# Kernel tuning notes

Hardware: AMD Instinct MI355X
Metric: run time of the kernel (lower is better)

The kernel has to match this reference:

```python
import jax, jax.numpy as jnp
import numpy as np

B, T, N, C, H, S = 8, 24, 2048, 64, 8, 4
HD = C // H
EPS_NORM = 1e-12   # torch F.normalize eps
EPS_DEN = 1e-5     # clamp_min in fast_attention
LN_EPS = 1e-5
SCALE1 = 0.01      # self.scale[1]


def _ln(x, g, b):
    m = x.mean(-1, keepdims=True)
    v = ((x - m) ** 2).mean(-1, keepdims=True)
    return (x - m) * jax.lax.rsqrt(v + LN_EPS) * g + b


def _fast_attn(q, k, v):
    # q,k,v: [b, l, h, m] ; performer-style linear attention with L2-normalized feature maps
    q = q / jnp.maximum(jnp.linalg.norm(q, axis=-1, keepdims=True), EPS_NORM)
    k = k / jnp.maximum(jnp.linalg.norm(k, axis=-1, keepdims=True), EPS_NORM)
    L = q.shape[1]
    kvs = jnp.einsum('blhm,blhd->bhmd', k, v)
    num = jnp.einsum('bnhm,bhmd->bnhd', q, kvs) + L * v
    den = jnp.einsum('bnhm,bhm->bnh', q, k.sum(axis=1))[..., None] + L
    return num / jnp.maximum(den, EPS_DEN)  # [b, l, h, d]


def _attn_layer(x, qkv_w, out_w, out_b):
    # x: [B, T, N, C]; spatial (over N) + temporal (over T) linear attention, concat, project
    b, t, n, c = x.shape
    qkv = x @ qkv_w.T                      # [b,t,n,3c], no bias (qkv_bias=False)
    q, k, v = jnp.split(qkv, 3, axis=-1)
    sh = lambda a: a.reshape(b * t, n, H, HD)                    # flatten (B,T) -> attend over nodes
    th = lambda a: a.swapaxes(1, 2).reshape(b * n, t, H, HD)     # flatten (B,N) -> attend over time
    out_s = _fast_attn(sh(q), sh(k), sh(v)).reshape(b, t, n, c)
    out_t = _fast_attn(th(q), th(k), th(v)).reshape(b, n, t, c).swapaxes(1, 2)
    return jnp.concatenate([out_s, out_t], axis=-1) @ out_w.T + out_b


def setup_inputs() -> dict:
    key = jax.random.key(0)
    ks = jax.random.split(key, 20)
    stdv = 1.0 / np.sqrt(N)
    w = 0.02
    inp = {
        'x': jax.random.normal(ks[0], (B, T, N, C), jnp.float32),
        'phi': jax.random.normal(ks[1], (S, N, N), jnp.float32) * (N ** -0.5),
        'phi_inv': jax.random.normal(ks[2], (S, N, N), jnp.float32) * (N ** -0.5),
        'diag_w': jax.random.uniform(ks[3], (S, N), jnp.float32, -stdv, stdv),
        'qkv0_w': jax.random.normal(ks[4], (3 * C, C), jnp.float32) * w,
        'out0_w': jax.random.normal(ks[5], (C, 2 * C), jnp.float32) * w,
        'out0_b': jnp.zeros((C,), jnp.float32),
        'qkv1_w': jax.random.normal(ks[6], (3 * C, C), jnp.float32) * w,
        'out1_w': jax.random.normal(ks[7], (C, 2 * C), jnp.float32) * w,
        'out1_b': jnp.zeros((C,), jnp.float32),
        'pw0_w': jax.random.normal(ks[8], (C, C), jnp.float32) * w,
        'pw0_b': jax.random.normal(ks[9], (C,), jnp.float32) * w,
        'pw1_w': jax.random.normal(ks[10], (C, C), jnp.float32) * w,
        'pw1_b': jax.random.normal(ks[11], (C,), jnp.float32) * w,
        'fc1_w': jax.random.normal(ks[12], (2 * C, C), jnp.float32) * w,
        'fc1_b': jnp.zeros((2 * C,), jnp.float32),
        'fc2_w': jax.random.normal(ks[13], (C, 2 * C), jnp.float32) * w,
        'fc2_b': jnp.zeros((C,), jnp.float32),
        'ln1_g': jnp.ones((C,), jnp.float32),
        'ln1_b': jnp.zeros((C,), jnp.float32),
        'ln2_g': jnp.ones((C,), jnp.float32),
        'ln2_b': jnp.zeros((C,), jnp.float32),
    }
    return inp


def reference(x, phi, phi_inv, diag_w, qkv0_w, out0_w, out0_b, qkv1_w, out1_w, out1_b,
              pw0_w, pw0_b, pw1_w, pw1_b, fc1_w, fc1_b, fc2_w, fc2_b,
              ln1_g, ln1_b, ln2_g, ln2_b):
    # Graph wavelet propagate (order=2): x_list = [x, W(x)] with
    # W(x)[b,t,n,c] = sum_j (sum_s phi_s diag(diag_w_s) phi_inv_s)[n,j] x[b,t,j,c]
    Msum = jnp.einsum('sij,sj,sjk->ik', phi, diag_w, phi_inv)   # [N,N]
    x_k = jnp.einsum('nj,btjc->btnc', Msum, x)
    att0 = _attn_layer(x, qkv0_w, out0_w, out0_b)
    att1 = _attn_layer(x_k, qkv1_w, out1_w, out1_b)
    # scale = [1, 0.01]; c starts as x, then becomes att0
    x_glo = x + att0 * (x @ pw0_w.T + pw0_b) + att1 * (att0 @ pw1_w.T + pw1_b) * SCALE1
    # In torch, x_glo aliases x (in-place +=), so ln1(x + x_glo) == ln1(2 * x_glo)
    y = _ln(2.0 * x_glo, ln1_g, ln1_b)
    h = jax.nn.relu(y @ fc1_w.T + fc1_b) @ fc2_w.T + fc2_b
    return _ln(y + h, ln2_g, ln2_b)
```

## Files before the change

kernel.cpp:

```cpp
#include <hip/hip_runtime.h>

typedef unsigned short u16;
typedef unsigned int u32;
typedef __attribute__((ext_vector_type(8))) __bf16 bf16x8;
typedef __attribute__((ext_vector_type(4))) float floatx4;

#define TB 24
#define NN 2048
#define QC 192

__device__ __forceinline__ float b2f(u16 v) { return __uint_as_float(((u32)v) << 16); }
__device__ __forceinline__ u16 f2bu(float f) {
  u32 u = __float_as_uint(f);
  u32 r = (u + 0x7fffu + ((u >> 16) & 1u)) >> 16;
  return (u16)r;
}
__device__ __forceinline__ u32 packpair(float a, float b) {
  return (u32)f2bu(a) | ((u32)f2bu(b) << 16);
}
__device__ __forceinline__ void unpack8(uint4 v, float* f) {
  f[0] = __uint_as_float(v.x << 16); f[1] = __uint_as_float(v.x & 0xffff0000u);
  f[2] = __uint_as_float(v.y << 16); f[3] = __uint_as_float(v.y & 0xffff0000u);
  f[4] = __uint_as_float(v.z << 16); f[5] = __uint_as_float(v.z & 0xffff0000u);
  f[6] = __uint_as_float(v.w << 16); f[7] = __uint_as_float(v.w & 0xffff0000u);
}
__device__ __forceinline__ float wredsum(float v) {
#pragma unroll
  for (int m = 32; m > 0; m >>= 1) v += __shfl_xor(v, m, 64);
  return v;
}
__device__ __forceinline__ float red16(float v) {
#pragma unroll
  for (int m = 8; m > 0; m >>= 1) v += __shfl_xor(v, m, 64);
  return v;
}

__global__ __launch_bounds__(256) void cast_weights(
    const float* __restrict__ q0, const float* __restrict__ q1,
    const float* __restrict__ o0, const float* __restrict__ o1,
    const float* __restrict__ p0, const float* __restrict__ p1,
    const float* __restrict__ f1, const float* __restrict__ f2,
    u16* __restrict__ dst) {
  int i = blockIdx.x * 256 + threadIdx.x;
  float v;
  if (i < 12288) v = q0[i];
  else if (i < 24576) v = q1[i - 12288];
  else if (i < 32768) v = o0[i - 24576];
  else if (i < 40960) v = o1[i - 32768];
  else if (i < 45056) v = p0[i - 40960];
  else if (i < 49152) v = p1[i - 45056];
  else if (i < 57344) v = f1[i - 49152];
  else v = f2[i - 57344];
  dst[i] = f2bu(v);
}

__global__ __launch_bounds__(256) void cast_bulk(const float* __restrict__ src,
                                                 u16* __restrict__ dst) {
  long i = ((long)blockIdx.x * 256 + threadIdx.x) * 8;
  float4 a = *(const float4*)(src + i);
  float4 b = *(const float4*)(src + i + 4);
  uint4 o = uint4{packpair(a.x, a.y), packpair(a.z, a.w),
                  packpair(b.x, b.y), packpair(b.z, b.w)};
  *(uint4*)(dst + i) = o;
}

__global__ __launch_bounds__(256) void prep_pt(const float* __restrict__ phi_inv,
                                               const float* __restrict__ diag,
                                               u16* __restrict__ PT) {
  const int s = blockIdx.z;
  const float* phi_inv_s = phi_inv + (long)s * 4194304;
  const float* diag_s = diag + (long)s * 2048;
  u16* PTs = PT + (long)s * 4194304;
  const long i0 = (long)blockIdx.x * 64, j0 = (long)blockIdx.y * 64;
  __shared__ float tile[64][65];
  for (int t = threadIdx.x; t < 512; t += 256) {
    int r = t >> 3, c8 = (t & 7) << 3;
    float dv = diag_s[j0 + r];
    const float* sp = phi_inv_s + (j0 + r) * 2048 + i0 + c8;
    float4 p = *(const float4*)sp;
    float4 q = *(const float4*)(sp + 4);
    tile[r][c8 + 0] = p.x * dv; tile[r][c8 + 1] = p.y * dv;
    tile[r][c8 + 2] = p.z * dv; tile[r][c8 + 3] = p.w * dv;
    tile[r][c8 + 4] = q.x * dv; tile[r][c8 + 5] = q.y * dv;
    tile[r][c8 + 6] = q.z * dv; tile[r][c8 + 7] = q.w * dv;
  }
  __syncthreads();
  for (int t = threadIdx.x; t < 512; t += 256) {
    int r = t >> 3, c8 = (t & 7) << 3;
    uint4 o;
    o.x = packpair(tile[c8 + 0][r], tile[c8 + 1][r]);
    o.y = packpair(tile[c8 + 2][r], tile[c8 + 3][r]);
    o.z = packpair(tile[c8 + 4][r], tile[c8 + 5][r]);
    o.w = packpair(tile[c8 + 6][r], tile[c8 + 7][r]);
    *(uint4*)(PTs + (i0 + r) * 2048 + j0 + c8) = o;
  }
}

__global__ __launch_bounds__(256) void prep_xt(const float* __restrict__ x,
                                               u16* __restrict__ XT,
                                               u16* __restrict__ XB) {
  const int bt = blockIdx.y;
  const long j0 = (long)blockIdx.x * 64;
  __shared__ float tile[64][65];
  const float* src = x + (long)bt * NN * 64;
  for (int t = threadIdx.x; t < 512; t += 256) {
    int r = t >> 3, c8 = (t & 7) << 3;
    const float* sp = src + (j0 + r) * 64 + c8;
    float4 p = *(const float4*)sp;
    float4 q = *(const float4*)(sp + 4);
    tile[r][c8 + 0] = p.x; tile[r][c8 + 1] = p.y;
    tile[r][c8 + 2] = p.z; tile[r][c8 + 3] = p.w;
    tile[r][c8 + 4] = q.x; tile[r][c8 + 5] = q.y;
    tile[r][c8 + 6] = q.z; tile[r][c8 + 7] = q.w;
    if (XB) {
      uint4 o = uint4{packpair(p.x, p.y), packpair(p.z, p.w),
                      packpair(q.x, q.y), packpair(q.z, q.w)};
      *(uint4*)(XB + (long)bt * 131072 + (j0 + r) * 64 + c8) = o;
    }
  }
  __syncthreads();
  u16* dst = XT + (long)bt * 64 * NN;
  for (int t = threadIdx.x; t < 512; t += 256) {
    int r = t >> 3, c8 = (t & 7) << 3;
    uint4 o;
    o.x = packpair(tile[c8 + 0][r], tile[c8 + 1][r]);
    o.y = packpair(tile[c8 + 2][r], tile[c8 + 3][r]);
    o.z = packpair(tile[c8 + 4][r], tile[c8 + 5][r]);
    o.w = packpair(tile[c8 + 6][r], tile[c8 + 7][r]);
    *(uint4*)(dst + (long)r * 2048 + j0 + c8) = o;
  }
}

template <int MODE>
__global__ __launch_bounds__(256) void gemm128(
    const u16* __restrict__ A, const u16* __restrict__ Bt, void* __restrict__ C,
    int K, int lda, int ldb, int ldc, int nseg, long aseg, long bseg) {
  __shared__ __align__(16) u16 As[128 * 64];
  __shared__ __align__(16) u16 Bs[128 * 64];
  const int tid = threadIdx.x;
  const int wave = tid >> 6, lane = tid & 63;
  const int l15 = lane & 15, lq = lane >> 4;
  const int wr = wave >> 1, wc = wave & 1;
  const int nbx = gridDim.x;
  const int nwg = nbx * gridDim.y;
  int id = blockIdx.x + nbx * blockIdx.y;
  id = (id & 7) * (nwg >> 3) + (id >> 3);
  const long m0 = (long)(id % nbx) * 128;
  const long n0 = (long)(id / nbx) * 128;
  const long zo = (MODE == 2) ? (long)blockIdx.z : 0;
  const int rl = lane >> 3;
  const int csw = (lane & 7) ^ rl;
  floatx4 acc[4][4];
#pragma unroll
  for (int a = 0; a < 4; a++)
#pragma unroll
    for (int b = 0; b < 4; b++) acc[a][b] = floatx4{0.f, 0.f, 0.f, 0.f};
  for (int s = 0; s < nseg; s++) {
    const u16* Ab = A + (s + zo) * aseg;
    const u16* Bb = Bt + (s + zo) * bseg;
    for (int k0 = 0; k0 < K; k0 += 64) {
      __syncthreads();
#pragma unroll
      for (int la = 0; la < 4; la++) {
        const int ldx = wave * 4 + la;
        const int rowt = ldx * 8 + rl;
        const u16* ga = Ab + (m0 + rowt) * (long)lda + k0 + csw * 8;
        const u16* gb = Bb + (n0 + rowt) * (long)ldb + k0 + csw * 8;
        __builtin_amdgcn_global_load_lds(
            (const __attribute__((address_space(1))) void*)ga,
            (__attribute__((address_space(3))) void*)(As + ldx * 512), 16, 0, 0);
        __builtin_amdgcn_global_load_lds(
            (const __attribute__((address_space(1))) void*)gb,
            (__attribute__((address_space(3))) void*)(Bs + ldx * 512), 16, 0, 0);
      }
      __syncthreads();
#pragma unroll
      for (int ks = 0; ks < 2; ks++) {
        bf16x8 af[4], bf[4];
        const int cp = ((ks * 4 + lq) ^ (l15 & 7)) * 8;
#pragma unroll
        for (int t = 0; t < 4; t++) {
          af[t] = *(const bf16x8*)(As + (wr * 64 + t * 16 + l15) * 64 + cp);
          bf[t] = *(const bf16x8*)(Bs + (wc * 64 + t * 16 + l15) * 64 + cp);
        }
#pragma unroll
        for (int ti = 0; ti < 4; ti++)
#pragma unroll
          for (int tj = 0; tj < 4; tj++)
            acc[ti][tj] = __builtin_amdgcn_mfma_f32_16x16x32_bf16(
                af[ti], bf[tj], acc[ti][tj], 0, 0, 0);
      }
    }
  }
#pragma unroll
  for (int ti = 0; ti < 4; ti++) {
#pragma unroll
    for (int tj = 0; tj < 4; tj++) {
#pragma unroll
      for (int i = 0; i < 4; i++) {
        const long row = m0 + wr * 64 + ti * 16 + lq * 4 + i;
        const long col = n0 + wc * 64 + tj * 16 + l15;
        if (MODE == 0) {
          ((u16*)C)[row * ldc + col] = f2bu(acc[ti][tj][i]);
        } else if (MODE == 1) {
          ((float*)C)[(col >> 6) * 131072L + row * 64 + (col & 63)] = acc[ti][tj][i];
        } else if (MODE == 2) {
          ((float*)C)[zo * 4194304L + row * (long)ldc + col] = acc[ti][tj][i];
        } else {
          ((u16*)C)[(col >> 6) * 131072L + row * 64 + (col & 63)] =
              f2bu(acc[ti][tj][i]);
        }
      }
    }
  }
}

__global__ __launch_bounds__(256) void reduce_ms(const float* __restrict__ P,
                                                 u16* __restrict__ M) {
  long i = ((long)blockIdx.x * 256 + threadIdx.x) * 8;
  float s[8];
  {
    float4 a = *(const float4*)(P + i);
    float4 b = *(const float4*)(P + i + 4);
    s[0] = a.x; s[1] = a.y; s[2] = a.z; s[3] = a.w;
    s[4] = b.x; s[5] = b.y; s[6] = b.z; s[7] = b.w;
  }
#pragma unroll
  for (int z = 1; z < 4; z++) {
    const float* p = P + (long)z * 4194304L + i;
    float4 a = *(const float4*)p;
    float4 b = *(const float4*)(p + 4);
    s[0] += a.x; s[1] += a.y; s[2] += a.z; s[3] += a.w;
    s[4] += b.x; s[5] += b.y; s[6] += b.z; s[7] += b.w;
  }
  uint4 o = uint4{packpair(s[0], s[1]), packpair(s[2], s[3]),
                  packpair(s[4], s[5]), packpair(s[6], s[7])};
  *(uint4*)(M + i) = o;
}

template <bool AF32, bool CF32>
__global__ __launch_bounds__(256) void gemm_bt(
    const void* __restrict__ A, const u16* __restrict__ Bt, void* __restrict__ C,
    int K, int lda, int ldb, int ldc, int nseg, long aseg, long bseg,
    long bbstride, long cbstride, int accum) {
  __shared__ __align__(16) u16 Asm[64][72];
  __shared__ __align__(16) u16 Bsm[64][72];
  const int tid = threadIdx.x;
  const int wave = tid >> 6, lane = tid & 63;
  const int l15 = lane & 15, lq = lane >> 4;
  const long m0 = (long)blockIdx.x * 64;
  const long n0 = (long)blockIdx.y * 64;
  const long bz = blockIdx.z;
  const int srow = tid >> 3;
  const int scol = (tid & 7) << 3;
  floatx4 acc[4];
#pragma unroll
  for (int t = 0; t < 4; t++) acc[t] = floatx4{0.f, 0.f, 0.f, 0.f};
  for (int s = 0; s < nseg; s++) {
    const u16* Bb = Bt + s * bseg + bz * bbstride;
    for (int k0 = 0; k0 < K; k0 += 64) {
      __syncthreads();
      uint4 a0, a1;
      if (AF32) {
        const float* Af = (const float*)A + s * aseg;
        const float* p0 = Af + (m0 + srow) * lda + k0 + scol;
        const float* p1 = Af + (m0 + srow + 32) * lda + k0 + scol;
        float4 x0 = *(const float4*)p0, x1 = *(const float4*)(p0 + 4);
        float4 y0 = *(const float4*)p1, y1 = *(const float4*)(p1 + 4);
        a0 = uint4{packpair(x0.x, x0.y), packpair(x0.z, x0.w),
                   packpair(x1.x, x1.y), packpair(x1.z, x1.w)};
        a1 = uint4{packpair(y0.x, y0.y), packpair(y0.z, y0.w),
                   packpair(y1.x, y1.y), packpair(y1.z, y1.w)};
      } else {
        const u16* Ab = (const u16*)A + s * aseg;
        a0 = *(const uint4*)(Ab + (m0 + srow) * lda + k0 + scol);
        a1 = *(const uint4*)(Ab + (m0 + srow + 32) * lda + k0 + scol);
      }
      uint4 b0 = *(const uint4*)(Bb + (n0 + srow) * ldb + k0 + scol);
      uint4 b1 = *(const uint4*)(Bb + (n0 + srow + 32) * ldb + k0 + scol);
      *(uint4*)(&Asm[srow][scol]) = a0;
      *(uint4*)(&Asm[srow + 32][scol]) = a1;
      *(uint4*)(&Bsm[srow][scol]) = b0;
      *(uint4*)(&Bsm[srow + 32][scol]) = b1;
      __syncthreads();
#pragma unroll
      for (int ks = 0; ks < 2; ks++) {
        bf16x8 af = *(const bf16x8*)(&Asm[wave * 16 + l15][ks * 32 + lq * 8]);
#pragma unroll
        for (int t = 0; t < 4; t++) {
          bf16x8 bfr = *(const bf16x8*)(&Bsm[t * 16 + l15][ks * 32 + lq * 8]);
          acc[t] = __builtin_amdgcn_mfma_f32_16x16x32_bf16(af, bfr, acc[t], 0, 0, 0);
        }
      }
    }
  }
#pragma unroll
  for (int t = 0; t < 4; t++) {
#pragma unroll
    for (int i = 0; i < 4; i++) {
      long off = (m0 + wave * 16 + lq * 4 + i) * ldc + n0 + t * 16 + l15;
      float v = acc[t][i];
      if (CF32) {
        float* Cb = (float*)C + bz * cbstride;
        if (accum) v += Cb[off];
        Cb[off] = v;
      } else {
        u16* Cb = (u16*)C + bz * cbstride;
        if (accum) v += b2f(Cb[off]);
        Cb[off] = f2bu(v);
      }
    }
  }
}

template <int K, int LDA, int NOUT, int LDO, bool BIAS, bool RELU, bool AF32, bool OF32>
__global__ __launch_bounds__(256) void skinny_gemm(const void* __restrict__ In,
                                                   const u16* __restrict__ W,
                                                   const float* __restrict__ Bv,
                                                   void* __restrict__ Out) {
  constexpr int NT = NOUT / 16;
  const int lane = threadIdx.x & 63;
  const int wave = threadIdx.x >> 6;
  const int l15 = lane & 15, lq = lane >> 4;
  const long m0 = ((long)blockIdx.x * 4 + wave) * 16;
  floatx4 acc[NT];
#pragma unroll
  for (int t = 0; t < NT; t++) acc[t] = floatx4{0.f, 0.f, 0.f, 0.f};
#pragma unroll
  for (int k0 = 0; k0 < K; k0 += 32) {
    bf16x8 af;
    if (AF32) {
      const float* arow = (const float*)In + (m0 + l15) * (long)LDA + lq * 8;
      float4 p = *(const float4*)(arow + k0);
      float4 q = *(const float4*)(arow + k0 + 4);
      uint4 pk = uint4{packpair(p.x, p.y), packpair(p.z, p.w),
                       packpair(q.x, q.y), packpair(q.z, q.w)};
      af = __builtin_bit_cast(bf16x8, pk);
    } else {
      const u16* arow = (const u16*)In + (m0 + l15) * (long)LDA + lq * 8;
      af = *(const bf16x8*)(arow + k0);
    }
#pragma unroll
    for (int t = 0; t < NT; t++) {
      bf16x8 bfr = *(const bf16x8*)(W + (t * 16 + l15) * K + k0 + lq * 8);
      acc[t] = __builtin_amdgcn_mfma_f32_16x16x32_bf16(af, bfr, acc[t], 0, 0, 0);
    }
  }
#pragma unroll
  for (int t = 0; t < NT; t++) {
    float bv = BIAS ? Bv[t * 16 + l15] : 0.f;
#pragma unroll
    for (int i = 0; i < 4; i++) {
      float v = acc[t][i] + bv;
      if (RELU) v = fmaxf(v, 0.f);
      long off = (m0 + lq * 4 + i) * (long)LDO + t * 16 + l15;
      if (OF32) ((float*)Out)[off] = v;
      else ((u16*)Out)[off] = f2bu(v);
    }
  }
}

__global__ __launch_bounds__(256) void spat_stats(const u16* __restrict__ Q,
                                                  float* __restrict__ stats) {
  const int nb = gridDim.x;
  int blk = blockIdx.x;
  const int bh = ((nb & 7) == 0) ? ((blk & 7) * (nb >> 3) + (blk >> 3)) : blk;
  const int bt = bh >> 3, h = bh & 7;
  const int tid = threadIdx.x, lane = tid & 63, wave = tid >> 6;
  float kvs[8][8], ksm[8];
#pragma unroll
  for (int m = 0; m < 8; m++) {
    ksm[m] = 0.f;
#pragma unroll
    for (int d = 0; d < 8; d++) kvs[m][d] = 0.f;
  }
  const u16* base = Q + (long)bt * NN * QC + 64 + h * 8;
  for (int l = tid; l < NN; l += 256) {
    const u16* p = base + (long)l * QC;
    float kv[8], vv[8];
    unpack8(*(const uint4*)p, kv);
    unpack8(*(const uint4*)(p + 64), vv);
    float nr = 0.f;
#pragma unroll
    for (int m = 0; m < 8; m++) nr += kv[m] * kv[m];
    float inv = 1.f / fmaxf(sqrtf(nr), 1e-12f);
#pragma unroll
    for (int m = 0; m < 8; m++) {
      float km = kv[m] * inv;
      ksm[m] += km;
#pragma unroll
      for (int d = 0; d < 8; d++) kvs[m][d] += km * vv[d];
    }
  }
  __shared__ float red[4][72];
#pragma unroll
  for (int m = 0; m < 8; m++) {
    ksm[m] = wredsum(ksm[m]);
#pragma unroll
    for (int d = 0; d < 8; d++) kvs[m][d] = wredsum(kvs[m][d]);
  }
  if (lane == 0) {
#pragma unroll
    for (int m = 0; m < 8; m++) {
      red[wave][64 + m] = ksm[m];
#pragma unroll
      for (int d = 0; d < 8; d++) red[wave][m * 8 + d] = kvs[m][d];
    }
  }
  __syncthreads();
  if (tid < 72) {
    stats[(long)bh * 72 + tid] = red[0][tid] + red[1][tid] + red[2][tid] + red[3][tid];
  }
}

__global__ __launch_bounds__(256) void temp_attn(u16* __restrict__ Q) {
  const long g = (long)blockIdx.x * 256 + threadIdx.x;
  const int h = (int)(g & 7);
  const long bn = g >> 3;
  const int n = (int)(bn & 2047);
  const int b = (int)(bn >> 11);
  u16* qb = Q + ((long)b * TB * NN + n) * QC + h * 8;
  const long ts = (long)NN * QC;
  float kvs[8][8], ksm[8];
#pragma unroll
  for (int m = 0; m < 8; m++) {
    ksm[m] = 0.f;
#pragma unroll
    for (int d = 0; d < 8; d++) kvs[m][d] = 0.f;
  }
  for (int t = 0; t < TB; t++) {
    const u16* p = qb + t * ts;
    float kv[8], vv[8];
    unpack8(*(const uint4*)(p + 64), kv);
    unpack8(*(const uint4*)(p + 128), vv);
    float nr = 0.f;
#pragma unroll
    for (int m = 0; m < 8; m++) nr += kv[m] * kv[m];
    float inv = 1.f / fmaxf(sqrtf(nr), 1e-12f);
#pragma unroll
    for (int m = 0; m < 8; m++) {
      float km = kv[m] * inv;
      ksm[m] += km;
#pragma unroll
      for (int d = 0; d < 8; d++) kvs[m][d] += km * vv[d];
    }
  }
  for (int t = 0; t < TB; t++) {
    u16* p = qb + t * ts;
    float qv[8], vv[8];
    unpack8(*(const uint4*)p, qv);
    unpack8(*(const uint4*)(p + 128), vv);
    float nr = 0.f;
#pragma unroll
    for (int m = 0; m < 8; m++) nr += qv[m] * qv[m];
    float inv = 1.f / fmaxf(sqrtf(nr), 1e-12f);
    float num[8];
    float den = 24.f;
#pragma unroll
    for (int d = 0; d < 8; d++) num[d] = 24.f * vv[d];
#pragma unroll
    for (int m = 0; m < 8; m++) {
      float qm = qv[m] * inv;
      den += qm * ksm[m];
#pragma unroll
      for (int d = 0; d < 8; d++) num[d] += qm * kvs[m][d];
    }
    den = fmaxf(den, 1e-5f);
    float id = 1.f / den;
    uint4 o;
    o.x = packpair(num[0] * id, num[1] * id);
    o.y = packpair(num[2] * id, num[3] * id);
    o.z = packpair(num[4] * id, num[5] * id);
    o.w = packpair(num[6] * id, num[7] * id);
    *(uint4*)(p + 64) = o;
  }
}

__global__ __launch_bounds__(256) void temp_spat(u16* __restrict__ Q,
                                                 const float* __restrict__ stats) {
  const long g = (long)blockIdx.x * 256 + threadIdx.x;
  const int h = (int)(g & 7);
  const long bn = g >> 3;
  const int n = (int)(bn & 2047);
  const int b = (int)(bn >> 11);
  u16* qb = Q + ((long)b * TB * NN + n) * QC + h * 8;
  const long ts = (long)NN * QC;
  float kvs[8][8], ksm[8];
#pragma unroll
  for (int m = 0; m < 8; m++) {
    ksm[m] = 0.f;
#pragma unroll
    for (int d = 0; d < 8; d++) kvs[m][d] = 0.f;
  }
  for (int t = 0; t < TB; t++) {
    const u16* p = qb + t * ts;
    float kv[8], vv[8];
    unpack8(*(const uint4*)(p + 64), kv);
    unpack8(*(const uint4*)(p + 128), vv);
    float nr = 0.f;
#pragma unroll
    for (int m = 0; m < 8; m++) nr += kv[m] * kv[m];
    float inv = 1.f / fmaxf(sqrtf(nr), 1e-12f);
#pragma unroll
    for (int m = 0; m < 8; m++) {
      float km = kv[m] * inv;
      ksm[m] += km;
#pragma unroll
      for (int d = 0; d < 8; d++) kvs[m][d] += km * vv[d];
    }
  }
  const float* stb = stats + ((long)b * TB * 8 + h) * 72;
  for (int t = 0; t < TB; t++) {
    u16* p = qb + t * ts;
    const float* st = stb + (long)t * 576;
    float qv[8], vv[8];
    unpack8(*(const uint4*)p, qv);
    unpack8(*(const uint4*)(p + 128), vv);
    float nr = 0.f;
#pragma unroll
    for (int m = 0; m < 8; m++) nr += qv[m] * qv[m];
    float inv = 1.f / fmaxf(sqrtf(nr), 1e-12f);
    float numt[8], nums[8];
    float dent = 24.f, dens = 2048.f;
#pragma unroll
    for (int d = 0; d < 8; d++) {
      numt[d] = 24.f * vv[d];
      nums[d] = 2048.f * vv[d];
    }
#pragma unroll
    for (int m = 0; m < 8; m++) {
      float qm = qv[m] * inv;
      dent += qm * ksm[m];
      dens += qm * st[64 + m];
#pragma unroll
      for (int d = 0; d < 8; d++) {
        numt[d] += qm * kvs[m][d];
        nums[d] += qm * st[m * 8 + d];
      }
    }
    float idt = 1.f / fmaxf(dent, 1e-5f);
    float ids = 1.f / fmaxf(dens, 1e-5f);
    uint4 os, ot;
    os.x = packpair(nums[0] * ids, nums[1] * ids);
    os.y = packpair(nums[2] * ids, nums[3] * ids);
    os.z = packpair(nums[4] * ids, nums[5] * ids);
    os.w = packpair(nums[6] * ids, nums[7] * ids);
    ot.x = packpair(numt[0] * idt, numt[1] * idt);
    ot.y = packpair(numt[2] * idt, numt[3] * idt);
    ot.z = packpair(numt[4] * idt, numt[5] * idt);
    ot.w = packpair(numt[6] * idt, numt[7] * idt);
    *(uint4*)p = os;
    *(uint4*)(p + 64) = ot;
  }
}

__global__ __launch_bounds__(256) void spat_out(u16* __restrict__ Q,
                                                const float* __restrict__ stats) {
  const long g = (long)blockIdx.x * 256 + threadIdx.x;
  const int h = (int)(g & 7);
  const long r = g >> 3;
  const int bt = (int)(r >> 11);
  u16* p = Q + r * QC + h * 8;
  float qv[8], vv[8];
  unpack8(*(const uint4*)p, qv);
  unpack8(*(const uint4*)(p + 128), vv);
  const float* st = stats + ((long)bt * 8 + h) * 72;
  float nr = 0.f;
#pragma unroll
  for (int m = 0; m < 8; m++) nr += qv[m] * qv[m];
  float inv = 1.f / fmaxf(sqrtf(nr), 1e-12f);
  const float L = 2048.f;
  float num[8];
#pragma unroll
  for (int d = 0; d < 8; d++) num[d] = L * vv[d];
  float den = L;
#pragma unroll
  for (int m = 0; m < 8; m++) {
    float qm = qv[m] * inv;
    den += qm * st[64 + m];
#pragma unroll
    for (int d = 0; d < 8; d++) num[d] += qm * st[m * 8 + d];
  }
  den = fmaxf(den, 1e-5f);
  float id = 1.f / den;
  uint4 o;
  o.x = packpair(num[0] * id, num[1] * id);
  o.y = packpair(num[2] * id, num[3] * id);
  o.z = packpair(num[4] * id, num[5] * id);
  o.w = packpair(num[6] * id, num[7] * id);
  *(uint4*)p = o;
}

__global__ __launch_bounds__(256) void pw1_combine_ln(
    const u16* __restrict__ Q, const u16* __restrict__ W,
    const float* __restrict__ Bv, const float* __restrict__ x,
    const u16* __restrict__ a1, const float* __restrict__ g1,
    const float* __restrict__ b1, u16* __restrict__ Y) {
  const int lane = threadIdx.x & 63;
  const int wave = threadIdx.x >> 6;
  const int l15 = lane & 15, lq = lane >> 4;
  const long m0 = ((long)blockIdx.x * 4 + wave) * 16;
  floatx4 acc[4];
#pragma unroll
  for (int t = 0; t < 4; t++) acc[t] = floatx4{0.f, 0.f, 0.f, 0.f};
#pragma unroll
  for (int k0 = 0; k0 < 64; k0 += 32) {
    bf16x8 af = *(const bf16x8*)(Q + (m0 + l15) * 192 + 128 + k0 + lq * 8);
#pragma unroll
    for (int t = 0; t < 4; t++) {
      bf16x8 bfr = *(const bf16x8*)(W + (t * 16 + l15) * 64 + k0 + lq * 8);
      acc[t] = __builtin_amdgcn_mfma_f32_16x16x32_bf16(af, bfr, acc[t], 0, 0, 0);
    }
  }
  float tv[4][4];
#pragma unroll
  for (int t = 0; t < 4; t++) {
    const int col = t * 16 + l15;
    const float bv = Bv[col];
#pragma unroll
    for (int i = 0; i < 4; i++) {
      const long row = m0 + lq * 4 + i;
      float p1v = acc[t][i] + bv;
      float xv = x[row * 64 + col];
      float a0 = b2f(Q[row * 192 + 128 + col]);
      float p0 = b2f(Q[row * 192 + col]);
      float a1v = b2f(a1[row * 64 + col]);
      tv[t][i] = 2.f * (xv + a0 * p0 + a1v * p1v * 0.01f);
    }
  }
#pragma unroll
  for (int i = 0; i < 4; i++) {
    float s = tv[0][i] + tv[1][i] + tv[2][i] + tv[3][i];
    s = red16(s);
    float mu = s * 0.015625f;
    float vs = 0.f;
#pragma unroll
    for (int t = 0; t < 4; t++) {
      float d = tv[t][i] - mu;
      vs += d * d;
    }
    vs = red16(vs);
    float rs = rsqrtf(vs * 0.015625f + 1e-5f);
    const long row = m0 + lq * 4 + i;
#pragma unroll
    for (int t = 0; t < 4; t++) {
      const int col = t * 16 + l15;
      float y = (tv[t][i] - mu) * rs * g1[col] + b1[col];
      Y[row * 64 + col] = f2bu(y);
    }
  }
}

__global__ __launch_bounds__(256) void fc2_ln(
    const u16* __restrict__ Hb, const u16* __restrict__ W,
    const float* __restrict__ Bv, const u16* __restrict__ Yb,
    const float* __restrict__ g2, const float* __restrict__ b2v,
    float* __restrict__ out) {
  const int lane = threadIdx.x & 63;
  const int wave = threadIdx.x >> 6;
  const int l15 = lane & 15, lq = lane >> 4;
  const long m0 = ((long)blockIdx.x * 4 + wave) * 16;
  floatx4 acc[4];
#pragma unroll
  for (int t = 0; t < 4; t++) acc[t] = floatx4{0.f, 0.f, 0.f, 0.f};
#pragma unroll
  for (int k0 = 0; k0 < 128; k0 += 32) {
    bf16x8 af = *(const bf16x8*)(Hb + (m0 + l15) * 128 + k0 + lq * 8);
#pragma unroll
    for (int t = 0; t < 4; t++) {
      bf16x8 bfr = *(const bf16x8*)(W + (t * 16 + l15) * 128 + k0 + lq * 8);
      acc[t] = __builtin_amdgcn_mfma_f32_16x16x32_bf16(af, bfr, acc[t], 0, 0, 0);
    }
  }
  float tv[4][4];
#pragma unroll
  for (int t = 0; t < 4; t++) {
    const int col = t * 16 + l15;
    const float bv = Bv[col];
#pragma unroll
    for (int i = 0; i < 4; i++) {
      const long row = m0 + lq * 4 + i;
      tv[t][i] = acc[t][i] + bv + b2f(Yb[row * 64 + col]);
    }
  }
#pragma unroll
  for (int i = 0; i < 4; i++) {
    float s = tv[0][i] + tv[1][i] + tv[2][i] + tv[3][i];
    s = red16(s);
    float mu = s * 0.015625f;
    float vs = 0.f;
#pragma unroll
    for (int t = 0; t < 4; t++) {
      float d = tv[t][i] - mu;
      vs += d * d;
    }
    vs = red16(vs);
    float rs = rsqrtf(vs * 0.015625f + 1e-5f);
    const long row = m0 + lq * 4 + i;
#pragma unroll
    for (int t = 0; t < 4; t++) {
      const int col = t * 16 + l15;
      out[row * 64 + col] = (tv[t][i] - mu) * rs * g2[col] + b2v[col];
    }
  }
}

__global__ __launch_bounds__(256) void combine_ln(
    const float* __restrict__ x, const u16* __restrict__ a0p, int sa0,
    const float* __restrict__ a1p, const u16* __restrict__ P0, int sp0,
    const u16* __restrict__ P1, int sp1, const float* __restrict__ g1,
    const float* __restrict__ b1, u16* __restrict__ Y) {
  const long r = (long)blockIdx.x * 4 + (threadIdx.x >> 6);
  const int d = threadIdx.x & 63;
  float xv = x[r * 64 + d];
  float a0 = b2f(a0p[r * sa0 + d]);
  float a1 = a1p[r * 64 + d];
  float p0 = b2f(P0[r * sp0 + d]);
  float p1 = b2f(P1[r * sp1 + d]);
  float t = 2.f * (xv + a0 * p0 + a1 * p1 * 0.01f);
  float mu = wredsum(t) * 0.015625f;
  float dv = t - mu;
  float var = wredsum(dv * dv) * 0.015625f;
  float y = dv * rsqrtf(var + 1e-5f) * g1[d] + b1[d];
  Y[r * 64 + d] = f2bu(y);
}

__global__ __launch_bounds__(256) void final_ln(const u16* __restrict__ Yp,
                                                const u16* __restrict__ Op,
                                                const float* __restrict__ g2,
                                                const float* __restrict__ b2p,
                                                float* __restrict__ out) {
  const long r = (long)blockIdx.x * 4 + (threadIdx.x >> 6);
  const int d = threadIdx.x & 63;
  const long o = r * 64 + d;
  float t = b2f(Yp[o]) + b2f(Op[o]);
  float mu = wredsum(t) * 0.015625f;
  float dv = t - mu;
  float var = wredsum(dv * dv) * 0.015625f;
  out[o] = dv * rsqrtf(var + 1e-5f) * g2[d] + b2p[d];
}

extern "C" void kernel_launch(void* const* d_in, const int* in_sizes, int n_in,
                              void* d_out, int out_size, void* d_ws, size_t ws_size,
                              hipStream_t stream) {
  const float* x = (const float*)d_in[0];
  const float* phi = (const float*)d_in[1];
  const float* phiinv = (const float*)d_in[2];
  const float* diagw = (const float*)d_in[3];
  const float* qkv0w = (const float*)d_in[4];
  const float* out0w = (const float*)d_in[5];
  const float* out0b = (const float*)d_in[6];
  const float* qkv1w = (const float*)d_in[7];
  const float* out1w = (const float*)d_in[8];
  const float* out1b = (const float*)d_in[9];
  const float* pw0w = (const float*)d_in[10];
  const float* pw0b = (const float*)d_in[11];
  const float* pw1w = (const float*)d_in[12];
  const float* pw1b = (const float*)d_in[13];
  const float* fc1w = (const float*)d_in[14];
  const float* fc1b = (const float*)d_in[15];
  const float* fc2w = (const float*)d_in[16];
  const float* fc2b = (const float*)d_in[17];
  const float* ln1g = (const float*)d_in[18];
  const float* ln1b = (const float*)d_in[19];
  const float* ln2g = (const float*)d_in[20];
  const float* ln2b = (const float*)d_in[21];

  const long per = 25221120L;
  int CH = 1;
  if ((long)ws_size >= 262144L + 8 * per) CH = 8;
  else if ((long)ws_size >= 262144L + 4 * per) CH = 4;
  else if ((long)ws_size >= 262144L + 2 * per) CH = 2;
  const int NCH = 8 / CH;

  char* ws = (char*)d_ws;
  u16* wb = (u16*)ws;
  u16* wq0 = wb + 0;
  u16* wq1 = wb + 12288;
  u16* wo0 = wb + 24576;
  u16* wo1 = wb + 32768;
  u16* wp0 = wb + 40960;
  u16* wp1 = wb + 45056;
  u16* wf1 = wb + 49152;
  u16* wf2 = wb + 57344;
  const long B0 = 262144L;
  float* dof = (float*)d_out;

  cast_weights<<<256, 256, 0, stream>>>(qkv0w, qkv1w, out0w, out1w, pw0w, pw1w,
                                        fc1w, fc2w, wb);

  if (CH == 8) {
    u16* PT = (u16*)(ws + B0);
    u16* PB = (u16*)(ws + B0 + 33554432L);
    float* MsP = (float*)(ws + B0 + 67108864L);
    u16* Ms = (u16*)(ws + B0 + 134217728L);
    u16* XT = (u16*)(ws + B0);
    u16* XB = (u16*)(ws + B0 + 151437312L);
    u16* Q = (u16*)(ws + B0);
    float* st = (float*)(ws + B0 + 150994944L);
    u16* Yb = XB;
    u16* Hb = (u16*)(ws + B0);
    u16* xkb = (u16*)d_out;
    u16* a1b = xkb + 25165824L;

    prep_pt<<<dim3(32, 32, 4), 256, 0, stream>>>(phiinv, diagw, PT);
    cast_bulk<<<8192, 256, 0, stream>>>(phi, PB);
    gemm128<2><<<dim3(16, 16, 4), 256, 0, stream>>>(PB, PT, MsP, 2048, 2048, 2048,
                                                    2048, 1, 4194304L, 4194304L);
    reduce_ms<<<2048, 256, 0, stream>>>(MsP, Ms);
    prep_xt<<<dim3(32, 192), 256, 0, stream>>>(x, XT, XB);
    gemm128<3><<<dim3(16, 96), 256, 0, stream>>>(Ms, XT, xkb, 2048, 2048, 2048, 0,
                                                 1, 0L, 0L);
    skinny_gemm<64, 64, 192, 192, false, false, false, false>
        <<<6144, 256, 0, stream>>>(xkb, wq1, nullptr, Q);
    spat_stats<<<1536, 256, 0, stream>>>(Q, st);
    temp_spat<<<512, 256, 0, stream>>>(Q, st);
    skinny_gemm<128, 192, 64, 64, true, false, false, false>
        <<<6144, 256, 0, stream>>>(Q, wo1, out1b, a1b);
    skinny_gemm<64, 64, 192, 192, false, false, false, false>
        <<<6144, 256, 0, stream>>>(XB, wq0, nullptr, Q);
    spat_stats<<<1536, 256, 0, stream>>>(Q, st);
    temp_spat<<<512, 256, 0, stream>>>(Q, st);
    skinny_gemm<128, 192, 64, 192, true, false, false, false>
        <<<6144, 256, 0, stream>>>(Q, wo0, out0b, Q + 128);
    skinny_gemm<64, 64, 64, 192, true, false, false, false>
        <<<6144, 256, 0, stream>>>(XB, wp0, pw0b, Q);
    pw1_combine_ln<<<6144, 256, 0, stream>>>(Q, wp1, pw1b, x, a1b, ln1g, ln1b, Yb);
    skinny_gemm<64, 64, 128, 128, true, true, false, false>
        <<<6144, 256, 0, stream>>>(Yb, wf1, fc1b, Hb);
    fc2_ln<<<6144, 256, 0, stream>>>(Hb, wf2, fc2b, Yb, ln2g, ln2b, dof);
  } else {
    u16* Ms = (u16*)(ws + B0);
    u16* PT = (u16*)(ws + B0 + 8388608L);
    u16* XT = (u16*)(ws + B0 + 8388608L);
    u16* Q = (u16*)(ws + B0);
    float* st = (float*)(ws + B0 + (long)CH * 18874368L);
    u16* Yb = (u16*)(ws + B0 + (long)CH * 18929664L);
    u16* Hb = (u16*)(ws + B0);
    u16* Ob = (u16*)(ws + B0 + (long)CH * 12582912L);

    for (int s = 0; s < 4; s++) {
      prep_pt<<<dim3(32, 32, 1), 256, 0, stream>>>(phiinv + (long)s * 4194304,
                                                   diagw + (long)s * 2048, PT);
      gemm_bt<true, false><<<dim3(32, 32, 1), 256, 0, stream>>>(
          phi + (long)s * 4194304, PT, Ms, 2048, 2048, 2048, 2048, 1, 0L, 0L, 0L,
          0L, s ? 1 : 0);
    }
    for (int c = 0; c < NCH; c++) {
      long eoff = (long)c * CH * 49152 * 64;
      prep_xt<<<dim3(32, CH * 24), 256, 0, stream>>>(x + eoff, XT, nullptr);
      gemm_bt<false, true><<<dim3(32, 1, CH * 24), 256, 0, stream>>>(
          Ms, XT, dof + eoff, 2048, 2048, 2048, 64, 1, 0L, 0L, 131072L, 131072L, 0);
    }
    for (int c = 0; c < NCH; c++) {
      long eoff = (long)c * CH * 49152 * 64;
      skinny_gemm<64, 64, 192, 192, false, false, true, false>
          <<<CH * 768, 256, 0, stream>>>(dof + eoff, wq1, nullptr, Q);
      spat_stats<<<CH * 192, 256, 0, stream>>>(Q, st);
      temp_attn<<<CH * 64, 256, 0, stream>>>(Q);
      spat_out<<<CH * 1536, 256, 0, stream>>>(Q, st);
      skinny_gemm<128, 192, 64, 64, true, false, false, true>
          <<<CH * 768, 256, 0, stream>>>(Q, wo1, out1b, dof + eoff);
    }
    for (int c = 0; c < NCH; c++) {
      long eoff = (long)c * CH * 49152 * 64;
      const float* x_c = x + eoff;
      skinny_gemm<64, 64, 192, 192, false, false, true, false>
          <<<CH * 768, 256, 0, stream>>>(x_c, wq0, nullptr, Q);
      spat_stats<<<CH * 192, 256, 0, stream>>>(Q, st);
      temp_attn<<<CH * 64, 256, 0, stream>>>(Q);
      spat_out<<<CH * 1536, 256, 0, stream>>>(Q, st);
      skinny_gemm<128, 192, 64, 192, true, false, false, false>
          <<<CH * 768, 256, 0, stream>>>(Q, wo0, out0b, Q + 128);
      skinny_gemm<64, 64, 64, 192, true, false, true, false>
          <<<CH * 768, 256, 0, stream>>>(x_c, wp0, pw0b, Q);
      skinny_gemm<64, 192, 64, 192, true, false, false, false>
          <<<CH * 768, 256, 0, stream>>>(Q + 128, wp1, pw1b, Q + 64);
      combine_ln<<<CH * 12288, 256, 0, stream>>>(x_c, Q + 128, 192, dof + eoff, Q,
                                                 192, Q + 64, 192, ln1g, ln1b, Yb);
      skinny_gemm<64, 64, 128, 128, true, true, false, false>
          <<<CH * 768, 256, 0, stream>>>(Yb, wf1, fc1b, Hb);
      skinny_gemm<128, 128, 64, 64, true, false, false, false>
          <<<CH * 768, 256, 0, stream>>>(Hb, wf2, fc2b, Ob);
      final_ln<<<CH * 12288, 256, 0, stream>>>(Yb, Ob, ln2g, ln2b, dof + eoff);
    }
  }
}
```

Measured before the change: 1.339 ms.

## Fuse tail GEMMs and LayerNorms into two kernels; remap temp_spat to wave-per-node

Five tail launches (out0 proj, pw0 proj, pw1+combine+LN1, fc1, fc2+LN2) become two kernels that keep intermediates (att0, fc1 hidden) in LDS per wave. This avoids writing and re-reading those activations through global memory. temp_spat now gives each node a whole wave with one output channel per lane, so each thread holds 8 accumulators instead of 72, with 8x more blocks. tail1 writes Y in place over XB, the same buffer it reads; this is safe only because each wave reads its own rows before writing them.

```diff
diff --git a/kernel.cpp b/kernel.cpp
--- a/kernel.cpp
+++ b/kernel.cpp
@@ -413,6 +413,81 @@
   }
 }
 
+__global__ __launch_bounds__(256) void temp_spat(u16* __restrict__ Q,
+                                                 const float* __restrict__ stats) {
+  const int wid = blockIdx.x * 4 + (threadIdx.x >> 6);
+  const int lane = threadIdx.x & 63;
+  const int h = lane >> 3, d = lane & 7;
+  const int n = wid & 2047;
+  const int b = wid >> 11;
+  u16* qb = Q + ((long)b * TB * NN + n) * QC;
+  const long ts = (long)NN * QC;
+  float kvsd[8], ksm[8];
+#pragma unroll
+  for (int m = 0; m < 8; m++) { kvsd[m] = 0.f; ksm[m] = 0.f; }
+  for (int tb = 0; tb < TB; tb += 4) {
+    uint4 kr[4]; u16 vr[4];
+#pragma unroll
+    for (int j = 0; j < 4; j++) {
+      const u16* p = qb + (long)(tb + j) * ts;
+      kr[j] = *(const uint4*)(p + 64 + h * 8);
+      vr[j] = p[128 + lane];
+    }
+#pragma unroll
+    for (int j = 0; j < 4; j++) {
+      float kv[8];
+      unpack8(kr[j], kv);
+      float vvd = b2f(vr[j]);
+      float nr = 0.f;
+#pragma unroll
+      for (int m = 0; m < 8; m++) nr += kv[m] * kv[m];
+      float inv = 1.f / fmaxf(sqrtf(nr), 1e-12f);
+#pragma unroll
+      for (int m = 0; m < 8; m++) {
+        float km = kv[m] * inv;
+        ksm[m] += km;
+        kvsd[m] += km * vvd;
+      }
+    }
+  }
+  const float* stb = stats + ((long)b * TB * 8 + h) * 72;
+  for (int tb = 0; tb < TB; tb += 4) {
+    uint4 qr[4]; u16 vr[4];
+#pragma unroll
+    for (int j = 0; j < 4; j++) {
+      const u16* p = qb + (long)(tb + j) * ts;
+      qr[j] = *(const uint4*)(p + h * 8);
+      vr[j] = p[128 + lane];
+    }
+#pragma unroll
+    for (int j = 0; j < 4; j++) {
+      const float* st = stb + (long)(tb + j) * 576;
+      float qv[8];
+      unpack8(qr[j], qv);
+      float vvd = b2f(vr[j]);
+      float nr = 0.f;
+#pragma unroll
+      for (int m = 0; m < 8; m++) nr += qv[m] * qv[m];
+      float inv = 1.f / fmaxf(sqrtf(nr), 1e-12f);
+      float numt = 24.f * vvd, nums = 2048.f * vvd;
+      float dent = 24.f, dens = 2048.f;
+#pragma unroll
+      for (int m = 0; m < 8; m++) {
+        float qm = qv[m] * inv;
+        dent += qm * ksm[m];
+        dens += qm * st[64 + m];
+        numt += qm * kvsd[m];
+        nums += qm * st[m * 8 + d];
+      }
+      float idt = 1.f / fmaxf(dent, 1e-5f);
+      float ids = 1.f / fmaxf(dens, 1e-5f);
+      u16* p = qb + (long)(tb + j) * ts;
+      p[lane] = f2bu(nums * ids);
+      p[64 + lane] = f2bu(numt * idt);
+    }
+  }
+}
+
 __global__ __launch_bounds__(256) void temp_attn(u16* __restrict__ Q) {
   const long g = (long)blockIdx.x * 256 + threadIdx.x;
   const int h = (int)(g & 7);
@@ -473,84 +548,6 @@
     o.z = packpair(num[4] * id, num[5] * id);
     o.w = packpair(num[6] * id, num[7] * id);
     *(uint4*)(p + 64) = o;
-  }
-}
-
-__global__ __launch_bounds__(256) void temp_spat(u16* __restrict__ Q,
-                                                 const float* __restrict__ stats) {
-  const long g = (long)blockIdx.x * 256 + threadIdx.x;
-  const int h = (int)(g & 7);
-  const long bn = g >> 3;
-  const int n = (int)(bn & 2047);
-  const int b = (int)(bn >> 11);
-  u16* qb = Q + ((long)b * TB * NN + n) * QC + h * 8;
-  const long ts = (long)NN * QC;
-  float kvs[8][8], ksm[8];
-#pragma unroll
-  for (int m = 0; m < 8; m++) {
-    ksm[m] = 0.f;
-#pragma unroll
-    for (int d = 0; d < 8; d++) kvs[m][d] = 0.f;
-  }
-  for (int t = 0; t < TB; t++) {
-    const u16* p = qb + t * ts;
-    float kv[8], vv[8];
-    unpack8(*(const uint4*)(p + 64), kv);
-    unpack8(*(const uint4*)(p + 128), vv);
-    float nr = 0.f;
-#pragma unroll
-    for (int m = 0; m < 8; m++) nr += kv[m] * kv[m];
-    float inv = 1.f / fmaxf(sqrtf(nr), 1e-12f);
-#pragma unroll
-    for (int m = 0; m < 8; m++) {
-      float km = kv[m] * inv;
-      ksm[m] += km;
-#pragma unroll
-      for (int d = 0; d < 8; d++) kvs[m][d] += km * vv[d];
-    }
-  }
-  const float* stb = stats + ((long)b * TB * 8 + h) * 72;
-  for (int t = 0; t < TB; t++) {
-    u16* p = qb + t * ts;
-    const float* st = stb + (long)t * 576;
-    float qv[8], vv[8];
-    unpack8(*(const uint4*)p, qv);
-    unpack8(*(const uint4*)(p + 128), vv);
-    float nr = 0.f;
-#pragma unroll
-    for (int m = 0; m < 8; m++) nr += qv[m] * qv[m];
-    float inv = 1.f / fmaxf(sqrtf(nr), 1e-12f);
-    float numt[8], nums[8];
-    float dent = 24.f, dens = 2048.f;
-#pragma unroll
-    for (int d = 0; d < 8; d++) {
-      numt[d] = 24.f * vv[d];
-      nums[d] = 2048.f * vv[d];
-    }
-#pragma unroll
-    for (int m = 0; m < 8; m++) {
-      float qm = qv[m] * inv;
-      dent += qm * ksm[m];
-      dens += qm * st[64 + m];
-#pragma unroll
-      for (int d = 0; d < 8; d++) {
-        numt[d] += qm * kvs[m][d];
-        nums[d] += qm * st[m * 8 + d];
-      }
-    }
-    float idt = 1.f / fmaxf(dent, 1e-5f);
-    float ids = 1.f / fmaxf(dens, 1e-5f);
-    uint4 os, ot;
-    os.x = packpair(nums[0] * ids, nums[1] * ids);
-    os.y = packpair(nums[2] * ids, nums[3] * ids);
-    os.z = packpair(nums[4] * ids, nums[5] * ids);
-    os.w = packpair(nums[6] * ids, nums[7] * ids);
-    ot.x = packpair(numt[0] * idt, numt[1] * idt);
-    ot.y = packpair(numt[2] * idt, numt[3] * idt);
-    ot.z = packpair(numt[4] * idt, numt[5] * idt);
-    ot.w = packpair(numt[6] * idt, numt[7] * idt);
-    *(uint4*)p = os;
-    *(uint4*)(p + 64) = ot;
   }
 }
 
@@ -591,11 +588,15 @@
   *(uint4*)p = o;
 }
 
-__global__ __launch_bounds__(256) void pw1_combine_ln(
-    const u16* __restrict__ Q, const u16* __restrict__ W,
-    const float* __restrict__ Bv, const float* __restrict__ x,
-    const u16* __restrict__ a1, const float* __restrict__ g1,
-    const float* __restrict__ b1, u16* __restrict__ Y) {
+__global__ __launch_bounds__(256) void tail1(
+    const u16* __restrict__ Q, const u16* __restrict__ XB,
+    const float* __restrict__ x, const u16* __restrict__ a1b,
+    const u16* __restrict__ wo0, const float* __restrict__ o0b,
+    const u16* __restrict__ wp0, const float* __restrict__ p0b,
+    const u16* __restrict__ wp1, const float* __restrict__ p1b,
+    const float* __restrict__ g1, const float* __restrict__ b1,
+    u16* __restrict__ Y) {
+  __shared__ u16 A0[4][16][72];
   const int lane = threadIdx.x & 63;
   const int wave = threadIdx.x >> 6;
   const int l15 = lane & 15, lq = lane >> 4;
@@ -604,28 +605,59 @@
 #pragma unroll
   for (int t = 0; t < 4; t++) acc[t] = floatx4{0.f, 0.f, 0.f, 0.f};
 #pragma unroll
+  for (int k0 = 0; k0 < 128; k0 += 32) {
+    bf16x8 af = *(const bf16x8*)(Q + (m0 + l15) * 192 + k0 + lq * 8);
+#pragma unroll
+    for (int t = 0; t < 4; t++) {
+      bf16x8 bfr = *(const bf16x8*)(wo0 + (t * 16 + l15) * 128 + k0 + lq * 8);
+      acc[t] = __builtin_amdgcn_mfma_f32_16x16x32_bf16(af, bfr, acc[t], 0, 0, 0);
+    }
+  }
+#pragma unroll
+  for (int t = 0; t < 4; t++) {
+    float bv = o0b[t * 16 + l15];
+#pragma unroll
+    for (int i = 0; i < 4; i++)
+      A0[wave][lq * 4 + i][t * 16 + l15] = f2bu(acc[t][i] + bv);
+  }
+  floatx4 ap0[4];
+#pragma unroll
+  for (int t = 0; t < 4; t++) ap0[t] = floatx4{0.f, 0.f, 0.f, 0.f};
+#pragma unroll
   for (int k0 = 0; k0 < 64; k0 += 32) {
-    bf16x8 af = *(const bf16x8*)(Q + (m0 + l15) * 192 + 128 + k0 + lq * 8);
+    bf16x8 af = *(const bf16x8*)(XB + (m0 + l15) * 64 + k0 + lq * 8);
 #pragma unroll
     for (int t = 0; t < 4; t++) {
-      bf16x8 bfr = *(const bf16x8*)(W + (t * 16 + l15) * 64 + k0 + lq * 8);
-      acc[t] = __builtin_amdgcn_mfma_f32_16x16x32_bf16(af, bfr, acc[t], 0, 0, 0);
+      bf16x8 bfr = *(const bf16x8*)(wp0 + (t * 16 + l15) * 64 + k0 + lq * 8);
+      ap0[t] = __builtin_amdgcn_mfma_f32_16x16x32_bf16(af, bfr, ap0[t], 0, 0, 0);
+    }
+  }
+  floatx4 ap1[4];
+#pragma unroll
+  for (int t = 0; t < 4; t++) ap1[t] = floatx4{0.f, 0.f, 0.f, 0.f};
+#pragma unroll
+  for (int k0 = 0; k0 < 64; k0 += 32) {
+    bf16x8 af = *(const bf16x8*)(&A0[wave][l15][k0 + lq * 8]);
+#pragma unroll
+    for (int t = 0; t < 4; t++) {
+      bf16x8 bfr = *(const bf16x8*)(wp1 + (t * 16 + l15) * 64 + k0 + lq * 8);
+      ap1[t] = __builtin_amdgcn_mfma_f32_16x16x32_bf16(af, bfr, ap1[t], 0, 0, 0);
     }
   }
   float tv[4][4];
 #pragma unroll
   for (int t = 0; t < 4; t++) {
     const int col = t * 16 + l15;
-    const float bv = Bv[col];
+    const float bp0 = p0b[col], bp1 = p1b[col];
 #pragma unroll
     for (int i = 0; i < 4; i++) {
       const long row = m0 + lq * 4 + i;
-      float p1v = acc[t][i] + bv;
       float xv = x[row * 64 + col];
-      float a0 = b2f(Q[row * 192 + 128 + col]);
-      float p0 = b2f(Q[row * 192 + col]);
-      float a1v = b2f(a1[row * 64 + col]);
-      tv[t][i] = 2.f * (xv + a0 * p0 + a1v * p1v * 0.01f);
+      float a0 = b2f(A0[wave][lq * 4 + i][col]);
+      float a1 = b2f(a1b[row * 64 + col]);
+      float p0v = ap0[t][i] + bp0;
+      float p1v = ap1[t][i] + bp1;
+      tv[t][i] = 2.f * (xv + a0 * p0v + a1 * p1v * 0.01f);
     }
   }
 #pragma unroll
@@ -636,8 +668,8 @@
     float vs = 0.f;
 #pragma unroll
     for (int t = 0; t < 4; t++) {
-      float d = tv[t][i] - mu;
-      vs += d * d;
+      float dd = tv[t][i] - mu;
+      vs += dd * dd;
     }
     vs = red16(vs);
     float rs = rsqrtf(vs * 0.015625f + 1e-5f);
@@ -651,48 +683,68 @@
   }
 }
 
-__global__ __launch_bounds__(256) void fc2_ln(
-    const u16* __restrict__ Hb, const u16* __restrict__ W,
-    const float* __restrict__ Bv, const u16* __restrict__ Yb,
-    const float* __restrict__ g2, const float* __restrict__ b2v,
-    float* __restrict__ out) {
+__global__ __launch_bounds__(256) void tail2(
+    const u16* __restrict__ Yb, const u16* __restrict__ wf1,
+    const float* __restrict__ f1b, const u16* __restrict__ wf2,
+    const float* __restrict__ fc2bv, const float* __restrict__ g2,
+    const float* __restrict__ b2v, float* __restrict__ out) {
+  __shared__ u16 HL[4][16][136];
   const int lane = threadIdx.x & 63;
   const int wave = threadIdx.x >> 6;
   const int l15 = lane & 15, lq = lane >> 4;
   const long m0 = ((long)blockIdx.x * 4 + wave) * 16;
-  floatx4 acc[4];
-#pragma unroll
-  for (int t = 0; t < 4; t++) acc[t] = floatx4{0.f, 0.f, 0.f, 0.f};
+  floatx4 acc1[8];
+#pragma unroll
+  for (int t = 0; t < 8; t++) acc1[t] = floatx4{0.f, 0.f, 0.f, 0.f};
+#pragma unroll
+  for (int k0 = 0; k0 < 64; k0 += 32) {
+    bf16x8 af = *(const bf16x8*)(Yb + (m0 + l15) * 64 + k0 + lq * 8);
+#pragma unroll
+    for (int t = 0; t < 8; t++) {
+      bf16x8 bfr = *(const bf16x8*)(wf1 + (t * 16 + l15) * 64 + k0 + lq * 8);
+      acc1[t] = __builtin_amdgcn_mfma_f32_16x16x32_bf16(af, bfr, acc1[t], 0, 0, 0);
+    }
+  }
+#pragma unroll
+  for (int t = 0; t < 8; t++) {
+    float bv = f1b[t * 16 + l15];
+#pragma unroll
+    for (int i = 0; i < 4; i++)
+      HL[wave][lq * 4 + i][t * 16 + l15] = f2bu(fmaxf(acc1[t][i] + bv, 0.f));
+  }
+  floatx4 acc2[4];
+#pragma unroll
+  for (int t = 0; t < 4; t++) acc2[t] = floatx4{0.f, 0.f, 0.f, 0.f};
 #pragma unroll
   for (int k0 = 0; k0 < 128; k0 += 32) {
-    bf16x8 af = *(const bf16x8*)(Hb + (m0 + l15) * 128 + k0 + lq * 8);
+    bf16x8 af = *(const bf16x8*)(&HL[wave][l15][k0 + lq * 8]);
 #pragma unroll
     for (int t = 0; t < 4; t++) {
-      bf16x8 bfr = *(const bf16x8*)(W + (t * 16 + l15) * 128 + k0 + lq * 8);
-      acc[t] = __builtin_amdgcn_mfma_f32_16x16x32_bf16(af, bfr, acc[t], 0, 0, 0);
-    }
-  }
-  float tv[4][4];
+      bf16x8 bfr = *(const bf16x8*)(wf2 + (t * 16 + l15) * 128 + k0 + lq * 8);
+      acc2[t] = __builtin_amdgcn_mfma_f32_16x16x32_bf16(af, bfr, acc2[t], 0, 0, 0);
+    }
+  }
+  float tw[4][4];
 #pragma unroll
   for (int t = 0; t < 4; t++) {
     const int col = t * 16 + l15;
-    const float bv = Bv[col];
+    const float bv = fc2bv[col];
 #pragma unroll
     for (int i = 0; i < 4; i++) {
       const long row = m0 + lq * 4 + i;
-      tv[t][i] = acc[t][i] + bv + b2f(Yb[row * 64 + col]);
+      tw[t][i] = acc2[t][i] + bv + b2f(Yb[row * 64 + col]);
     }
   }
 #pragma unroll
   for (int i = 0; i < 4; i++) {
-    float s = tv[0][i] + tv[1][i] + tv[2][i] + tv[3][i];
+    float s = tw[0][i] + tw[1][i] + tw[2][i] + tw[3][i];
     s = red16(s);
     float mu = s * 0.015625f;
     float vs = 0.f;
 #pragma unroll
     for (int t = 0; t < 4; t++) {
-      float d = tv[t][i] - mu;
-      vs += d * d;
+      float dd = tw[t][i] - mu;
+      vs += dd * dd;
     }
     vs = red16(vs);
     float rs = rsqrtf(vs * 0.015625f + 1e-5f);
@@ -700,7 +752,7 @@
 #pragma unroll
     for (int t = 0; t < 4; t++) {
       const int col = t * 16 + l15;
-      out[row * 64 + col] = (tv[t][i] - mu) * rs * g2[col] + b2v[col];
+      out[row * 64 + col] = (tw[t][i] - mu) * rs * g2[col] + b2v[col];
     }
   }
 }
@@ -798,8 +850,6 @@
     u16* XB = (u16*)(ws + B0 + 151437312L);
     u16* Q = (u16*)(ws + B0);
     float* st = (float*)(ws + B0 + 150994944L);
-    u16* Yb = XB;
-    u16* Hb = (u16*)(ws + B0);
     u16* xkb = (u16*)d_out;
     u16* a1b = xkb + 25165824L;
 
@@ -814,21 +864,16 @@
     skinny_gemm<64, 64, 192, 192, false, false, false, false>
         <<<6144, 256, 0, stream>>>(xkb, wq1, nullptr, Q);
     spat_stats<<<1536, 256, 0, stream>>>(Q, st);
-    temp_spat<<<512, 256, 0, stream>>>(Q, st);
+    temp_spat<<<4096, 256, 0, stream>>>(Q, st);
     skinny_gemm<128, 192, 64, 64, true, false, false, false>
         <<<6144, 256, 0, stream>>>(Q, wo1, out1b, a1b);
     skinny_gemm<64, 64, 192, 192, false, false, false, false>
         <<<6144, 256, 0, stream>>>(XB, wq0, nullptr, Q);
     spat_stats<<<1536, 256, 0, stream>>>(Q, st);
-    temp_spat<<<512, 256, 0, stream>>>(Q, st);
-    skinny_gemm<128, 192, 64, 192, true, false, false, false>
-        <<<6144, 256, 0, stream>>>(Q, wo0, out0b, Q + 128);
-    skinny_gemm<64, 64, 64, 192, true, false, false, false>
-        <<<6144, 256, 0, stream>>>(XB, wp0, pw0b, Q);
-    pw1_combine_ln<<<6144, 256, 0, stream>>>(Q, wp1, pw1b, x, a1b, ln1g, ln1b, Yb);
-    skinny_gemm<64, 64, 128, 128, true, true, false, false>
-        <<<6144, 256, 0, stream>>>(Yb, wf1, fc1b, Hb);
-    fc2_ln<<<6144, 256, 0, stream>>>(Hb, wf2, fc2b, Yb, ln2g, ln2b, dof);
+    temp_spat<<<4096, 256, 0, stream>>>(Q, st);
+    tail1<<<6144, 256, 0, stream>>>(Q, XB, x, a1b, wo0, out0b, wp0, pw0b, wp1,
+                                    pw1b, ln1g, ln1b, XB);
+    tail2<<<6144, 256, 0, stream>>>(XB, wf1, fc1b, wf2, fc2b, ln2g, ln2b, dof);
   } else {
     u16* Ms = (u16*)(ws + B0);
     u16* PT = (u16*)(ws + B0 + 8388608L);
```

Result: no change. 1.353 ms (+1.0%).
